# Optimization experiments

Measured on AMD Instinct MI355X. Metric: run time of the kernel, lower is better.

The kernel has to match this reference:

```python
import jax, jax.numpy as jnp
import numpy as np

N = 8192      # nodes (N_features)
D = 64        # oscillator dimension
E_K = 262144  # Kuramoto coupling edges
E_HK = 262144 # Hopfield-Kuramoto coupling edges
H = 64        # interaction MLP hidden width (N_weights)
KAPPA_K = 2.0
KAPPA_H = 2.0


def setup_inputs() -> dict:
    key = jax.random.key(0)
    ks = jax.random.split(key, 9)
    return dict(
        state_H=jax.random.normal(ks[0], (N,), dtype=jnp.float32),
        state_K=jax.random.normal(ks[1], (N, D), dtype=jnp.float32),
        W_H=jax.random.normal(ks[2], (N, N), dtype=jnp.float32) / np.float32(np.sqrt(N)),
        omega=jax.random.normal(ks[3], (D, D), dtype=jnp.float32),
        w1=jax.random.normal(ks[4], (1, H), dtype=jnp.float32),
        b1=jnp.zeros((H,), dtype=jnp.float32),
        w2=jax.random.normal(ks[5], (H, 1), dtype=jnp.float32) / np.float32(np.sqrt(H)),
        ind_K=jax.random.randint(ks[6], (E_K, 2), 0, N),
        ind_HK=jax.random.randint(ks[7], (E_HK, 2), 0, N),
    )


def _interaction_K(s, w1, b1, w2):
    # edgewise scalar MLP: [E] -> [E], dE/ds of the Kuramoto interaction energy
    h = jnp.tanh(s[:, None] @ w1 + b1)  # [E, H]
    return (h @ w2)[:, 0]               # [E]


def reference(state_H, state_K, W_H, omega, w1, b1, w2, ind_K, ind_HK):
    # normalize oscillator states onto unit sphere (per node)
    state_K = state_K / jnp.linalg.norm(state_K, axis=1, keepdims=True)

    i, j = ind_HK[:, 0], ind_HK[:, 1]
    Gram = jnp.sum(state_K[i] * state_K[j], axis=1)  # [E_HK]

    # Hopfield model: g = LNet.get_g(state_H), f_H = Hopfield_model(t, state_H, ...)
    g = jnp.tanh(state_H)                 # [N]
    f_H = -state_H + W_H @ g              # [N] dense Hopfield dynamics
    f_H = f_H.at[i].add(Gram * g[j] / KAPPA_H)
    f_H = f_H.at[j].add(Gram * g[i] / KAPPA_H)

    # Kuramoto edge coupling
    p, q = ind_K[:, 0], ind_K[:, 1]
    s = jnp.sum(state_K[p] * state_K[q], axis=1)        # [E_K]
    dE_ds = _interaction_K(s, w1, b1, w2)[:, None]      # [E_K, 1]
    f_K = jnp.zeros_like(state_K)
    f_K = f_K.at[p].add(dE_ds * state_K[q])
    f_K = f_K.at[q].add(dE_ds * state_K[p])

    # Hopfield->Kuramoto coupling
    G = (g[i] * g[j])[:, None]                          # [E_HK, 1]
    f_K = f_K.at[i].add(-G * state_K[j] / KAPPA_K)
    f_K = f_K.at[j].add(-G * state_K[i] / KAPPA_K)

    # project onto tangent of the sphere + antisymmetric rotation
    f_K = (-f_K
           + state_K * jnp.sum(state_K * f_K, axis=1, keepdims=True)
           + state_K @ ((omega - omega.T) * 0.5))
    return (f_H, f_K)
```

## Files before the change

### kernel.cpp

```cpp
#include <hip/hip_runtime.h>
#include <math.h>

#define N 8192
#define D 64
#define E_K 262144
#define E_HK 262144
#define NEDGE (E_K + E_HK)
#define CAP 256
#define TAB_N 2048
#define BATCH 8

constexpr float INV_KAPPA = 0.5f;

__device__ inline float fast_tanh(float x) {
  x = fminf(15.f, fmaxf(-15.f, x));
  float e = __expf(2.f * x);
  return (e - 1.f) * __builtin_amdgcn_rcpf(e + 1.f);
}

__device__ inline float wave_reduce(float v) {
  #pragma unroll
  for (int off = 32; off > 0; off >>= 1) v += __shfl_xor(v, off);
  return v;
}

__global__ __launch_bounds__(256) void prep_scatter_kernel(
    const float* __restrict__ state_K, const float* __restrict__ state_H,
    const float* __restrict__ omega,
    const int* __restrict__ ind_HK, const int* __restrict__ ind_K,
    const float* __restrict__ w1, const float* __restrict__ b1,
    const float* __restrict__ w2,
    float* __restrict__ Knorm, float* __restrict__ g, float* __restrict__ Om,
    float* __restrict__ Tab, int* __restrict__ cursor,
    int* __restrict__ entries) {
  int b = blockIdx.x;
  if (b < 2048) {
    int t = b * 256 + threadIdx.x;
    int i, j, bit;
    if (t < E_HK) {
      int2 e = ((const int2*)ind_HK)[t];
      i = e.x; j = e.y; bit = (int)0x80000000;
    } else {
      int2 e = ((const int2*)ind_K)[t - E_HK];
      i = e.x; j = e.y; bit = 0;
    }
    int s0 = atomicAdd(&cursor[i], 1);
    if (s0 < CAP) entries[i * CAP + s0] = j | bit;
    int s1 = atomicAdd(&cursor[j], 1);
    if (s1 < CAP) entries[j * CAP + s1] = i | bit;
  } else if (b < 4096) {
    int lane = threadIdx.x & 63;
    int row  = (b - 2048) * 4 + (threadIdx.x >> 6);
    float v  = state_K[row * D + lane];
    float ss = wave_reduce(v * v);
    Knorm[row * D + lane] = v * __builtin_amdgcn_rcpf(sqrtf(ss));
    if (lane == 0) g[row] = fast_tanh(state_H[row]);
  } else if (b == 4096) {
    for (int t = threadIdx.x; t < D * D; t += 256) {
      int a = t >> 6, c = t & 63;
      Om[t] = 0.5f * (omega[a * D + c] - omega[c * D + a]);
    }
  } else {
    int lane = threadIdx.x & 63;
    int p = (b - 4097) * 4 + (threadIdx.x >> 6);
    if (p <= TAB_N) {
      float s = (float)p * (2.0f / TAB_N) - 1.0f;
      float t = fast_tanh(s * w1[lane] + b1[lane]) * w2[lane];
      t = wave_reduce(t);
      if (lane == 0) Tab[p] = t;
    }
  }
}

__global__ __launch_bounds__(256) void mega_kernel(
    const float* __restrict__ W_H, const float* __restrict__ state_H,
    const float* __restrict__ Knorm, const float* __restrict__ g,
    const float* __restrict__ Om, const float* __restrict__ Tab,
    const int* __restrict__ cursor, const int* __restrict__ entries,
    float* __restrict__ f_H, float* __restrict__ f_K) {
  int row  = blockIdx.x;
  int lane = threadIdx.x & 63;
  int wv   = threadIdx.x >> 6;

  const float4* Wrow = reinterpret_cast<const float4*>(W_H + (size_t)row * N);
  float4 wreg[8];
  #pragma unroll
  for (int k = 0; k < 8; ++k) wreg[k] = Wrow[threadIdx.x + k * 256];

  float kr = Knorm[row * D + lane];
  float gr = g[row];

  __shared__ int   sh_ent[CAP];
  __shared__ float sTab[TAB_N + 1];
  int len = min(cursor[row], CAP);
  for (int e = threadIdx.x; e < len; e += 256)
    sh_ent[e] = entries[row * CAP + e];
  for (int t = threadIdx.x; t <= TAB_N; t += 256)
    sTab[t] = Tab[t];
  __syncthreads();

  float acc  = 0.f;
  float accH = 0.f;
  for (int base = wv * BATCH; base < len; base += 4 * BATCH) {
    int   ents[BATCH];
    float kov[BATCH], dv[BATCH];
    #pragma unroll
    for (int k = 0; k < BATCH; ++k) {
      if (base + k < len) {
        ents[k] = sh_ent[base + k];
        kov[k]  = Knorm[(size_t)(ents[k] & 0x7FFFFFFF) * D + lane];
      } else { ents[k] = 0; kov[k] = 0.f; }
    }
    #pragma unroll
    for (int k = 0; k < BATCH; ++k) dv[k] = kr * kov[k];
    #pragma unroll
    for (int off = 32; off > 0; off >>= 1) {
      #pragma unroll
      for (int k = 0; k < BATCH; ++k) dv[k] += __shfl_xor(dv[k], off);
    }
    #pragma unroll
    for (int k = 0; k < BATCH; ++k) {
      int ent = ents[k];
      if (ent < 0) {
        float go = g[ent & 0x7FFFFFFF];
        acc  += (-gr * go * INV_KAPPA) * kov[k];
        accH += go * kov[k];
      } else {
        float x = fminf(fmaxf((dv[k] + 1.0f) * (TAB_N * 0.5f), 0.0f),
                        (float)TAB_N);
        int   i  = min((int)x, TAB_N - 1);
        float fr = x - (float)i;
        float de = sTab[i] + (sTab[i + 1] - sTab[i]) * fr;
        acc += de * kov[k];
      }
    }
  }

  const float4* g4 = reinterpret_cast<const float4*>(g);
  float mv = 0.f;
  #pragma unroll
  for (int k = 0; k < 8; ++k) {
    float4 gg = g4[threadIdx.x + k * 256];
    mv += wreg[k].x * gg.x + wreg[k].y * gg.y +
          wreg[k].z * gg.z + wreg[k].w * gg.w;
  }
  mv = wave_reduce(mv);

  __shared__ float sAcc[4][D];
  __shared__ float sAccH[4][D];
  __shared__ float sMv[4];
  sAcc[wv][lane]  = acc;
  sAccH[wv][lane] = accH;
  if (lane == 0) sMv[wv] = mv;
  __syncthreads();

  if (wv == 0) {
    float tot  = sAcc[0][lane] + sAcc[1][lane] + sAcc[2][lane] + sAcc[3][lane];
    float totH = sAccH[0][lane] + sAccH[1][lane] + sAccH[2][lane] + sAccH[3][lane];
    float rd = wave_reduce(kr * tot);
    float sh = wave_reduce(kr * totH);
    float krot = 0.f;
    #pragma unroll
    for (int d = 0; d < D; ++d)
      krot += __shfl(kr, d) * Om[d * D + lane];
    f_K[row * D + lane] = -tot + kr * rd + krot;
    if (lane == 0)
      f_H[row] = -state_H[row] + sMv[0] + sMv[1] + sMv[2] + sMv[3]
                 + sh * INV_KAPPA;
  }
}

extern "C" void kernel_launch(void* const* d_in, const int* in_sizes, int n_in,
                              void* d_out, int out_size, void* d_ws, size_t ws_size,
                              hipStream_t stream) {
  const float* state_H = (const float*)d_in[0];
  const float* state_K = (const float*)d_in[1];
  const float* W_H     = (const float*)d_in[2];
  const float* omega   = (const float*)d_in[3];
  const float* w1      = (const float*)d_in[4];
  const float* b1      = (const float*)d_in[5];
  const float* w2      = (const float*)d_in[6];
  const int*   ind_K   = (const int*)d_in[7];
  const int*   ind_HK  = (const int*)d_in[8];

  float* f_H = (float*)d_out;
  float* f_K = (float*)d_out + N;

  char* ws = (char*)d_ws;
  int*   entries = (int*)ws;               ws += (size_t)N * CAP * sizeof(int);
  float* Knorm   = (float*)ws;             ws += (size_t)N * D * sizeof(float);
  float* g       = (float*)ws;             ws += N * sizeof(float);
  float* Om      = (float*)ws;             ws += D * D * sizeof(float);
  float* Tab     = (float*)ws;             ws += (TAB_N + 1) * sizeof(float);
  int*   cursor  = (int*)ws;

  hipMemsetAsync(cursor, 0, N * sizeof(int), stream);
  prep_scatter_kernel<<<4097 + 513, 256, 0, stream>>>(
      state_K, state_H, omega, ind_HK, ind_K, w1, b1, w2,
      Knorm, g, Om, Tab, cursor, entries);
  mega_kernel<<<N, 256, 0, stream>>>(W_H, state_H, Knorm, g, Om, Tab,
                                     cursor, entries, f_H, f_K);
}
```

Baseline: 505.3 us.

## Compute per-edge coefficients once in a separate kernel, split matvec from gather

Replaces the single mega kernel with two kernels. The first runs the dense W_H matvec alongside a per-edge pass that computes each edge's dot product and MLP coefficient once. The second gathers neighbours using packed entries that hold the neighbour index and the edge id, instead of recomputing every dot product twice per edge with wave reductions. This removes the duplicated dot-product and table work, but adds a kernel launch and a coefficient buffer round trip through memory, and the entry packing assumes edge ids below 2^19.

```diff
diff --git a/kernel.cpp b/kernel.cpp
--- a/kernel.cpp
+++ b/kernel.cpp
@@ -8,9 +8,6 @@
 #define NEDGE (E_K + E_HK)
 #define CAP 256
 #define TAB_N 2048
-#define BATCH 8
-
-constexpr float INV_KAPPA = 0.5f;
 
 __device__ inline float fast_tanh(float x) {
   x = fminf(15.f, fmaxf(-15.f, x));
@@ -32,22 +29,17 @@
     const float* __restrict__ w2,
     float* __restrict__ Knorm, float* __restrict__ g, float* __restrict__ Om,
     float* __restrict__ Tab, int* __restrict__ cursor,
-    int* __restrict__ entries) {
+    unsigned* __restrict__ entries) {
   int b = blockIdx.x;
   if (b < 2048) {
     int t = b * 256 + threadIdx.x;
-    int i, j, bit;
-    if (t < E_HK) {
-      int2 e = ((const int2*)ind_HK)[t];
-      i = e.x; j = e.y; bit = (int)0x80000000;
-    } else {
-      int2 e = ((const int2*)ind_K)[t - E_HK];
-      i = e.x; j = e.y; bit = 0;
-    }
+    int2 e = (t < E_HK) ? ((const int2*)ind_HK)[t]
+                        : ((const int2*)ind_K)[t - E_HK];
+    unsigned i = (unsigned)e.x, j = (unsigned)e.y;
     int s0 = atomicAdd(&cursor[i], 1);
-    if (s0 < CAP) entries[i * CAP + s0] = j | bit;
+    if (s0 < CAP) entries[i * CAP + s0] = (j << 19) | (unsigned)t;
     int s1 = atomicAdd(&cursor[j], 1);
-    if (s1 < CAP) entries[j * CAP + s1] = i | bit;
+    if (s1 < CAP) entries[j * CAP + s1] = (i << 19) | (unsigned)t;
   } else if (b < 4096) {
     int lane = threadIdx.x & 63;
     int row  = (b - 2048) * 4 + (threadIdx.x >> 6);
@@ -72,101 +64,102 @@
   }
 }
 
-__global__ __launch_bounds__(256) void mega_kernel(
-    const float* __restrict__ W_H, const float* __restrict__ state_H,
+__global__ __launch_bounds__(256) void matvec_coeff_kernel(
+    const float* __restrict__ W_H, const float* __restrict__ g,
+    const float* __restrict__ state_H, const float* __restrict__ Knorm,
+    const float* __restrict__ Tab,
+    const int* __restrict__ ind_HK, const int* __restrict__ ind_K,
+    float* __restrict__ f_H, float* __restrict__ coeff) {
+  int b    = blockIdx.x;
+  int lane = threadIdx.x & 63;
+  int wv   = threadIdx.x >> 6;
+  __shared__ float sbuf[4];
+  if (b < N) {
+    int row = b;
+    const float4* Wrow = reinterpret_cast<const float4*>(W_H + (size_t)row * N);
+    const float4* g4   = reinterpret_cast<const float4*>(g);
+    float acc = 0.0f;
+    #pragma unroll
+    for (int c = threadIdx.x; c < N / 4; c += 256) {
+      float4 w = Wrow[c];
+      float4 gg = g4[c];
+      acc += w.x * gg.x + w.y * gg.y + w.z * gg.z + w.w * gg.w;
+    }
+    acc = wave_reduce(acc);
+    if (lane == 0) sbuf[wv] = acc;
+    __syncthreads();
+    if (threadIdx.x == 0)
+      f_H[row] = -state_H[row] + sbuf[0] + sbuf[1] + sbuf[2] + sbuf[3];
+  } else {
+    int wid = (b - N) * 4 + wv;
+    int2 e = (wid < E_HK) ? ((const int2*)ind_HK)[wid]
+                          : ((const int2*)ind_K)[wid - E_HK];
+    float kp = Knorm[e.x * D + lane];
+    float kq = Knorm[e.y * D + lane];
+    float s = wave_reduce(kp * kq);
+    float c = s;
+    if (wid >= E_HK) {
+      float x = fminf(fmaxf((s + 1.0f) * (TAB_N * 0.5f), 0.0f), (float)TAB_N);
+      int   i  = min((int)x, TAB_N - 1);
+      float fr = x - (float)i;
+      c = Tab[i] + (Tab[i + 1] - Tab[i]) * fr;
+    }
+    if (lane == 0) coeff[wid] = c;
+  }
+}
+
+__global__ __launch_bounds__(256) void gather_kernel(
     const float* __restrict__ Knorm, const float* __restrict__ g,
-    const float* __restrict__ Om, const float* __restrict__ Tab,
-    const int* __restrict__ cursor, const int* __restrict__ entries,
+    const float* __restrict__ Om, const float* __restrict__ coeff,
+    const int* __restrict__ cursor, const unsigned* __restrict__ entries,
     float* __restrict__ f_H, float* __restrict__ f_K) {
   int row  = blockIdx.x;
   int lane = threadIdx.x & 63;
   int wv   = threadIdx.x >> 6;
-
-  const float4* Wrow = reinterpret_cast<const float4*>(W_H + (size_t)row * N);
-  float4 wreg[8];
-  #pragma unroll
-  for (int k = 0; k < 8; ++k) wreg[k] = Wrow[threadIdx.x + k * 256];
-
   float kr = Knorm[row * D + lane];
   float gr = g[row];
+  int len  = min(cursor[row], CAP);
 
-  __shared__ int   sh_ent[CAP];
-  __shared__ float sTab[TAB_N + 1];
-  int len = min(cursor[row], CAP);
-  for (int e = threadIdx.x; e < len; e += 256)
-    sh_ent[e] = entries[row * CAP + e];
-  for (int t = threadIdx.x; t <= TAB_N; t += 256)
-    sTab[t] = Tab[t];
-  __syncthreads();
+  int slot = lane * 4 + wv;
+  unsigned myent = (unsigned)E_HK;
+  float myc = 0.f, myg = 0.f;
+  if (slot < len) {
+    myent = entries[(size_t)row * CAP + slot];
+    myc   = coeff[myent & 0x7FFFFu];
+    myg   = g[myent >> 19];
+  }
+  int nl = (len > wv) ? min(64, (len - wv + 3) >> 2) : 0;
 
-  float acc  = 0.f;
-  float accH = 0.f;
-  for (int base = wv * BATCH; base < len; base += 4 * BATCH) {
-    int   ents[BATCH];
-    float kov[BATCH], dv[BATCH];
+  float acc = 0.f, sH = 0.f;
+  for (int k = 0; k < nl; k += 4) {
     #pragma unroll
-    for (int k = 0; k < BATCH; ++k) {
-      if (base + k < len) {
-        ents[k] = sh_ent[base + k];
-        kov[k]  = Knorm[(size_t)(ents[k] & 0x7FFFFFFF) * D + lane];
-      } else { ents[k] = 0; kov[k] = 0.f; }
-    }
-    #pragma unroll
-    for (int k = 0; k < BATCH; ++k) dv[k] = kr * kov[k];
-    #pragma unroll
-    for (int off = 32; off > 0; off >>= 1) {
-      #pragma unroll
-      for (int k = 0; k < BATCH; ++k) dv[k] += __shfl_xor(dv[k], off);
-    }
-    #pragma unroll
-    for (int k = 0; k < BATCH; ++k) {
-      int ent = ents[k];
-      if (ent < 0) {
-        float go = g[ent & 0x7FFFFFFF];
-        acc  += (-gr * go * INV_KAPPA) * kov[k];
-        accH += go * kov[k];
-      } else {
-        float x = fminf(fmaxf((dv[k] + 1.0f) * (TAB_N * 0.5f), 0.0f),
-                        (float)TAB_N);
-        int   i  = min((int)x, TAB_N - 1);
-        float fr = x - (float)i;
-        float de = sTab[i] + (sTab[i + 1] - sTab[i]) * fr;
-        acc += de * kov[k];
-      }
+    for (int u = 0; u < 4; ++u) {
+      unsigned ent = (unsigned)__shfl((int)myent, k + u);
+      float c  = __shfl(myc, k + u);
+      float go = __shfl(myg, k + u);
+      unsigned oth = ent >> 19;
+      bool hk = (ent & 0x7FFFFu) < (unsigned)E_HK;
+      float ko = Knorm[oth * D + lane];
+      acc += (hk ? (-gr * go * 0.5f) : c) * ko;
+      sH  += hk ? c * go : 0.f;
     }
   }
 
-  const float4* g4 = reinterpret_cast<const float4*>(g);
-  float mv = 0.f;
-  #pragma unroll
-  for (int k = 0; k < 8; ++k) {
-    float4 gg = g4[threadIdx.x + k * 256];
-    mv += wreg[k].x * gg.x + wreg[k].y * gg.y +
-          wreg[k].z * gg.z + wreg[k].w * gg.w;
-  }
-  mv = wave_reduce(mv);
-
   __shared__ float sAcc[4][D];
-  __shared__ float sAccH[4][D];
-  __shared__ float sMv[4];
-  sAcc[wv][lane]  = acc;
-  sAccH[wv][lane] = accH;
-  if (lane == 0) sMv[wv] = mv;
+  __shared__ float sHs[4];
+  sAcc[wv][lane] = acc;
+  if (lane == 0) sHs[wv] = sH;
   __syncthreads();
-
   if (wv == 0) {
-    float tot  = sAcc[0][lane] + sAcc[1][lane] + sAcc[2][lane] + sAcc[3][lane];
-    float totH = sAccH[0][lane] + sAccH[1][lane] + sAccH[2][lane] + sAccH[3][lane];
+    float tot = sAcc[0][lane] + sAcc[1][lane] + sAcc[2][lane] + sAcc[3][lane];
     float rd = wave_reduce(kr * tot);
-    float sh = wave_reduce(kr * totH);
     float krot = 0.f;
     #pragma unroll
     for (int d = 0; d < D; ++d)
       krot += __shfl(kr, d) * Om[d * D + lane];
     f_K[row * D + lane] = -tot + kr * rd + krot;
     if (lane == 0)
-      f_H[row] = -state_H[row] + sMv[0] + sMv[1] + sMv[2] + sMv[3]
-                 + sh * INV_KAPPA;
+      f_H[row] += (sHs[0] + sHs[1] + sHs[2] + sHs[3]) * 0.5f;
   }
 }
 
@@ -187,17 +180,20 @@
   float* f_K = (float*)d_out + N;
 
   char* ws = (char*)d_ws;
-  int*   entries = (int*)ws;               ws += (size_t)N * CAP * sizeof(int);
-  float* Knorm   = (float*)ws;             ws += (size_t)N * D * sizeof(float);
-  float* g       = (float*)ws;             ws += N * sizeof(float);
-  float* Om      = (float*)ws;             ws += D * D * sizeof(float);
-  float* Tab     = (float*)ws;             ws += (TAB_N + 1) * sizeof(float);
-  int*   cursor  = (int*)ws;
+  unsigned* entries = (unsigned*)ws;     ws += (size_t)N * CAP * sizeof(unsigned);
+  float* Knorm  = (float*)ws;            ws += (size_t)N * D * sizeof(float);
+  float* coeff  = (float*)ws;            ws += (size_t)NEDGE * sizeof(float);
+  float* g      = (float*)ws;            ws += N * sizeof(float);
+  float* Om     = (float*)ws;            ws += D * D * sizeof(float);
+  float* Tab    = (float*)ws;            ws += (TAB_N + 1) * sizeof(float);
+  int*   cursor = (int*)ws;
 
   hipMemsetAsync(cursor, 0, N * sizeof(int), stream);
   prep_scatter_kernel<<<4097 + 513, 256, 0, stream>>>(
       state_K, state_H, omega, ind_HK, ind_K, w1, b1, w2,
       Knorm, g, Om, Tab, cursor, entries);
-  mega_kernel<<<N, 256, 0, stream>>>(W_H, state_H, Knorm, g, Om, Tab,
-                                     cursor, entries, f_H, f_K);
+  matvec_coeff_kernel<<<N + NEDGE / 4, 256, 0, stream>>>(
+      W_H, g, state_H, Knorm, Tab, ind_HK, ind_K, f_H, coeff);
+  gather_kernel<<<N, 256, 0, stream>>>(Knorm, g, Om, coeff, cursor, entries,
+                                       f_H, f_K);
 }
```

After: 563.2 us. 1.11x slower.
